# Performance work log

Hardware: AMD Instinct MI355X
Metric: run time of the kernel (lower is better)

Reference implementation:

```python
import jax, jax.numpy as jnp
import numpy as np

B, L, N = 4, 1024, 2048
V_DIM, L_DIM, HID, H = 512, 768, 512, 8
HD = HID // H
SCALE = HD ** -0.5


def setup_inputs() -> dict:
    key = jax.random.key(0)
    ks = jax.random.split(key, 6)
    return {
        "x": jax.random.normal(ks[0], (B, L, V_DIM), dtype=jnp.float32),
        "vfeats": jax.random.normal(ks[1], (B, N, L_DIM), dtype=jnp.float32),
        "topk_mask": jax.random.normal(ks[2], (B, H, L, N), dtype=jnp.float32),
        "Wq": jax.random.normal(ks[3], (HID, V_DIM), dtype=jnp.float32) * 0.02,
        "Wkv": jax.random.normal(ks[4], (2 * HID, L_DIM), dtype=jnp.float32) * 0.02,
        "Wproj": jax.random.normal(ks[5], (V_DIM, HID), dtype=jnp.float32) * 0.02,
        "bproj": jnp.zeros((V_DIM,), dtype=jnp.float32),
    }


def reference(x, vfeats, topk_mask, Wq, Wkv, Wproj, bproj):
    # q: [B,L,HID] -> [B,H,L,HD]
    q = (x @ Wq.T).reshape(B, L, H, HD).transpose(0, 2, 1, 3)
    # kv: [B,N,2*HID] -> k,v each [B,H,N,HD]
    kv = (vfeats @ Wkv.T).reshape(B, N, 2, H, HD).transpose(2, 0, 3, 1, 4)
    k, v = kv[0], kv[1]
    attn = jnp.einsum("bhld,bhnd->bhln", q, k) * SCALE + topk_mask
    attn = jax.nn.softmax(attn, axis=-1)
    out = jnp.einsum("bhln,bhnd->bhld", attn, v)  # [B,H,L,HD]
    out = out.transpose(0, 2, 1, 3).reshape(B, L, HID)
    return out @ Wproj.T + bproj
```

## Files before the change

kernel.cpp:

```cpp
#include <hip/hip_runtime.h>
#include <math.h>

#define B_ 4
#define L_ 1024
#define N_ 2048
#define VDIM_ 512
#define LDIM_ 768
#define HID_ 512
#define H_ 8
#define HD_ 64
#define SCALE_ 0.125f

typedef __bf16 bf16;
typedef __bf16 bf16x4 __attribute__((ext_vector_type(4)));
typedef __bf16 bf16x8 __attribute__((ext_vector_type(8)));
typedef float f32x4 __attribute__((ext_vector_type(4)));

__device__ __forceinline__ void async_cp16(const bf16* g, bf16* l) {
    __builtin_amdgcn_global_load_lds(
        (const __attribute__((address_space(1))) unsigned int*)g,
        (__attribute__((address_space(3))) unsigned int*)l, 16, 0, 0);
}

#define XE_   2097152
#define VFE_  6291456
#define WQE_  262144
#define WKVE_ 786432
__global__ void cvt_all(const float* __restrict__ x, const float* __restrict__ vf,
                        const float* __restrict__ wq, const float* __restrict__ wkv,
                        bf16* __restrict__ xb, bf16* __restrict__ vfb,
                        bf16* __restrict__ wqb, bf16* __restrict__ wkvb)
{
    int e = (blockIdx.x * 256 + threadIdx.x) * 4;
    const float* src; bf16* dst; int off;
    if (e < XE_)                        { src = x;   dst = xb;   off = 0; }
    else if (e < XE_ + VFE_)            { src = vf;  dst = vfb;  off = XE_; }
    else if (e < XE_ + VFE_ + WQE_)     { src = wq;  dst = wqb;  off = XE_ + VFE_; }
    else                                { src = wkv; dst = wkvb; off = XE_ + VFE_ + WQE_; }
    int i = e - off;
    float4 v = *(const float4*)(src + i);
    bf16x4 o;
    o[0] = (bf16)v.x; o[1] = (bf16)v.y; o[2] = (bf16)v.z; o[3] = (bf16)v.w;
    *(bf16x4*)(dst + i) = o;
}

__global__ void cvt_split(const float* __restrict__ in, bf16* __restrict__ hi,
                          bf16* __restrict__ lo, int n) {
    int i = (blockIdx.x * 256 + threadIdx.x) * 4;
    if (i < n) {
        float4 v = *(const float4*)(in + i);
        bf16x4 h, lw;
        float vv[4] = {v.x, v.y, v.z, v.w};
        #pragma unroll
        for (int j = 0; j < 4; ++j) {
            bf16 hb = (bf16)vv[j];
            h[j] = hb;
            lw[j] = (bf16)(vv[j] - (float)hb);
        }
        *(bf16x4*)(hi + i) = h;
        *(bf16x4*)(lo + i) = lw;
    }
}

template<int BM, int BN>
__global__ __launch_bounds__(256)
void gemm_bf16(const bf16* __restrict__ A, const bf16* __restrict__ W,
               bf16* __restrict__ C, int M, int N, int K)
{
    __shared__ bf16 As[BM * 64];
    __shared__ bf16 Ws[BN * 64];
    const int t = threadIdx.x, l = t & 63, wv = t >> 6;
    const int n0 = blockIdx.x * BN, m0 = blockIdx.y * BM;
    const int wm = (wv >> 1) * (BM / 2), wn = (wv & 1) * (BN / 2);
    constexpr int TI = BM / 32, TJ = BN / 32;
    const int lq = l & 15, qd = l >> 4, swz = l & 7;

    f32x4 acc[TI][TJ];
    #pragma unroll
    for (int i = 0; i < TI; ++i)
        #pragma unroll
        for (int j = 0; j < TJ; ++j)
            #pragma unroll
            for (int r = 0; r < 4; ++r) acc[i][j][r] = 0.f;

    for (int kt = 0; kt < K; kt += 64) {
        __syncthreads();
        for (int it = wv; it < BM / 8; it += 4) {
            int r = it * 8 + (l >> 3);
            int c = (l & 7) ^ (r & 7);
            async_cp16(A + (size_t)(m0 + r) * K + kt + c * 8, &As[it * 512]);
        }
        for (int it = wv; it < BN / 8; it += 4) {
            int r = it * 8 + (l >> 3);
            int c = (l & 7) ^ (r & 7);
            async_cp16(W + (size_t)(n0 + r) * K + kt + c * 8, &Ws[it * 512]);
        }
        __syncthreads();
        #pragma unroll
        for (int ks = 0; ks < 2; ++ks) {
            bf16x8 af[TI], wf[TJ];
            #pragma unroll
            for (int i = 0; i < TI; ++i) {
                int row = wm + i * 16 + lq;
                af[i] = *(const bf16x8*)&As[row * 64 + ((ks * 4 + qd) ^ swz) * 8];
            }
            #pragma unroll
            for (int j = 0; j < TJ; ++j) {
                int row = wn + j * 16 + lq;
                wf[j] = *(const bf16x8*)&Ws[row * 64 + ((ks * 4 + qd) ^ swz) * 8];
            }
            #pragma unroll
            for (int i = 0; i < TI; ++i)
                #pragma unroll
                for (int j = 0; j < TJ; ++j)
                    acc[i][j] = __builtin_amdgcn_mfma_f32_16x16x32_bf16(
                        af[i], wf[j], acc[i][j], 0, 0, 0);
        }
    }
    #pragma unroll
    for (int i = 0; i < TI; ++i)
        #pragma unroll
        for (int j = 0; j < TJ; ++j)
            #pragma unroll
            for (int r = 0; r < 4; ++r) {
                int row = m0 + wm + i * 16 + qd * 4 + r;
                int col = n0 + wn + j * 16 + lq;
                C[(size_t)row * N + col] = (bf16)acc[i][j][r];
            }
}

__global__ __launch_bounds__(256)
void gemm_proj(const bf16* __restrict__ A, const bf16* __restrict__ Wh,
               const bf16* __restrict__ Wl, const float* __restrict__ bias,
               float* __restrict__ Cf, int M, int N, int K)
{
    __shared__ bf16 sA[64 * 64];
    __shared__ bf16 sWh[64 * 64], sWl[64 * 64];
    const int t = threadIdx.x, l = t & 63, wv = t >> 6;
    const int n0 = blockIdx.x * 64, m0 = blockIdx.y * 64;
    const int wm = (wv >> 1) * 32, wn = (wv & 1) * 32;
    const int lq = l & 15, qd = l >> 4, swz = l & 7;

    f32x4 acc[2][2];
    #pragma unroll
    for (int i = 0; i < 2; ++i)
        #pragma unroll
        for (int j = 0; j < 2; ++j)
            #pragma unroll
            for (int r = 0; r < 4; ++r) acc[i][j][r] = 0.f;

    for (int kt = 0; kt < K; kt += 64) {
        __syncthreads();
        for (int it = wv; it < 8; it += 4) {
            int r = it * 8 + (l >> 3);
            int c = (l & 7) ^ (r & 7);
            async_cp16(A  + (size_t)(m0 + r) * K + kt + c * 8, &sA[it * 512]);
            size_t go = (size_t)(n0 + r) * K + kt + c * 8;
            async_cp16(Wh + go, &sWh[it * 512]);
            async_cp16(Wl + go, &sWl[it * 512]);
        }
        __syncthreads();
        #pragma unroll
        for (int ks = 0; ks < 2; ++ks) {
            bf16x8 af[2], wh[2], wl[2];
            #pragma unroll
            for (int i = 0; i < 2; ++i) {
                int off = (wm + i * 16 + lq) * 64 + ((ks * 4 + qd) ^ swz) * 8;
                af[i] = *(const bf16x8*)&sA[off];
            }
            #pragma unroll
            for (int j = 0; j < 2; ++j) {
                int off = (wn + j * 16 + lq) * 64 + ((ks * 4 + qd) ^ swz) * 8;
                wh[j] = *(const bf16x8*)&sWh[off];
                wl[j] = *(const bf16x8*)&sWl[off];
            }
            #pragma unroll
            for (int i = 0; i < 2; ++i)
                #pragma unroll
                for (int j = 0; j < 2; ++j) {
                    acc[i][j] = __builtin_amdgcn_mfma_f32_16x16x32_bf16(af[i], wh[j], acc[i][j], 0, 0, 0);
                    acc[i][j] = __builtin_amdgcn_mfma_f32_16x16x32_bf16(af[i], wl[j], acc[i][j], 0, 0, 0);
                }
        }
    }
    #pragma unroll
    for (int i = 0; i < 2; ++i)
        #pragma unroll
        for (int j = 0; j < 2; ++j) {
            int col = n0 + wn + j * 16 + lq;
            float bb = bias[col];
            #pragma unroll
            for (int r = 0; r < 4; ++r) {
                int row = m0 + wm + i * 16 + qd * 4 + r;
                Cf[(size_t)row * N + col] = acc[i][j][r] + bb;
            }
        }
}

__global__ __launch_bounds__(256)
void transpose_v(const bf16* __restrict__ kv, bf16* __restrict__ vT)
{
    __shared__ bf16 T[64 * 64];
    const int t = threadIdx.x;
    const int bid = blockIdx.x;
    const int nt = bid & 31, h = (bid >> 5) & 7, b = bid >> 8;
    const int n0 = nt * 64;
    for (int g = t; g < 512; g += 256) {
        int r = g >> 3, c = g & 7;
        bf16x8 v = *(const bf16x8*)(kv + (size_t)(b * N_ + n0 + r) * (2 * HID_) +
                                    HID_ + h * HD_ + c * 8);
        *(bf16x8*)&T[r * 64 + (c ^ (r & 7)) * 8] = v;
    }
    __syncthreads();
    for (int g = t; g < 512; g += 256) {
        int d = g >> 3, kg = g & 7;
        bf16x8 ov;
        #pragma unroll
        for (int jj = 0; jj < 8; ++jj) {
            int key = kg * 8 + jj;
            ov[jj] = T[key * 64 + (((d >> 3) ^ (key & 7))) * 8 + (d & 7)];
        }
        *(bf16x8*)&vT[(size_t)((b * H_ + h) * HD_ + d) * N_ + n0 + kg * 8] = ov;
    }
}

#define PST 136
__global__ __launch_bounds__(256)
void attn_mfma(const bf16* __restrict__ q, const bf16* __restrict__ kv,
               const bf16* __restrict__ vT, const float* __restrict__ mask,
               bf16* __restrict__ ao)
{
    __shared__ bf16 Ks[128 * 64];
    __shared__ bf16 Vs[64 * 128];
    __shared__ bf16 Pa[4][16 * PST];
    const int t = threadIdx.x, l = t & 63, wv = t >> 6;
    const int bid = blockIdx.x;
    const int lt = bid & 15, h = (bid >> 4) & 7, b = bid >> 7;
    const int l0 = lt * 64;
    const int lq = l & 15, qd = l >> 4, swz = l & 7;

    bf16x8 qf[2];
    {
        const bf16* qb = q + (size_t)(b * L_ + l0 + wv * 16 + lq) * HID_ + h * HD_ + qd * 8;
        qf[0] = *(const bf16x8*)qb;
        qf[1] = *(const bf16x8*)(qb + 32);
    }

    f32x4 o[4];
    #pragma unroll
    for (int j = 0; j < 4; ++j)
        #pragma unroll
        for (int r = 0; r < 4; ++r) o[j][r] = 0.f;
    float m_run[4], l_run[4];
    #pragma unroll
    for (int r = 0; r < 4; ++r) { m_run[r] = -1e30f; l_run[r] = 0.f; }

    const bf16* kb = kv + (size_t)(b * N_) * (2 * HID_) + h * HD_;
    const bf16* vb = vT + (size_t)((b * H_ + h) * HD_) * N_;
    const size_t mrow0 = (size_t)((b * H_ + h) * L_ + l0 + wv * 16);
    bf16* Paw = &Pa[wv][0];

    for (int nt = 0; nt < N_ / 128; ++nt) {
        const int n0 = nt * 128;
        __syncthreads();
        float mk[8][4];
        #pragma unroll
        for (int jj = 0; jj < 8; ++jj)
            #pragma unroll
            for (int r = 0; r < 4; ++r)
                mk[jj][r] = mask[(mrow0 + qd * 4 + r) * N_ + n0 + jj * 16 + lq];
        for (int it = wv; it < 16; it += 4) {
            int r = it * 8 + (l >> 3);
            int c = (l & 7) ^ (r & 7);
            async_cp16(kb + (size_t)(n0 + r) * (2 * HID_) + c * 8, &Ks[it * 512]);
        }
        for (int it = wv; it < 16; it += 4) {
            int r = it * 4 + (l >> 4);
            int c = (l & 15) ^ (r & 15);
            async_cp16(vb + (size_t)r * N_ + n0 + c * 8, &Vs[it * 512]);
        }
        __syncthreads();
        f32x4 s[8];
        #pragma unroll
        for (int jj = 0; jj < 8; ++jj)
            #pragma unroll
            for (int r = 0; r < 4; ++r) s[jj][r] = 0.f;
        #pragma unroll
        for (int ks = 0; ks < 2; ++ks)
            #pragma unroll
            for (int jj = 0; jj < 8; ++jj) {
                bf16x8 kf = *(const bf16x8*)&Ks[(jj * 16 + lq) * 64 +
                                                ((ks * 4 + qd) ^ swz) * 8];
                s[jj] = __builtin_amdgcn_mfma_f32_16x16x32_bf16(qf[ks], kf, s[jj], 0, 0, 0);
            }
        #pragma unroll
        for (int jj = 0; jj < 8; ++jj)
            #pragma unroll
            for (int r = 0; r < 4; ++r)
                s[jj][r] = fmaf(s[jj][r], SCALE_, mk[jj][r]);
        float alpha[4], mnew[4];
        #pragma unroll
        for (int r = 0; r < 4; ++r) {
            float mx = s[0][r];
            #pragma unroll
            for (int jj = 1; jj < 8; ++jj) mx = fmaxf(mx, s[jj][r]);
            #pragma unroll
            for (int d2 = 1; d2 < 16; d2 <<= 1) mx = fmaxf(mx, __shfl_xor(mx, d2));
            mnew[r] = fmaxf(m_run[r], mx);
            alpha[r] = __expf(m_run[r] - mnew[r]);
            m_run[r] = mnew[r];
        }
        bf16 pb[8][4];
        #pragma unroll
        for (int r = 0; r < 4; ++r) {
            float ss = 0.f;
            #pragma unroll
            for (int jj = 0; jj < 8; ++jj) {
                float p = __expf(s[jj][r] - mnew[r]);
                pb[jj][r] = (bf16)p;
                ss += p;
            }
            #pragma unroll
            for (int d2 = 1; d2 < 16; d2 <<= 1) ss += __shfl_xor(ss, d2);
            l_run[r] = l_run[r] * alpha[r] + ss;
        }
        #pragma unroll
        for (int jj = 0; jj < 8; ++jj)
            #pragma unroll
            for (int r = 0; r < 4; ++r)
                Paw[(qd * 4 + r) * PST + jj * 16 + lq] = pb[jj][r];
        __asm__ __volatile__("s_waitcnt lgkmcnt(0)" ::: "memory");
        #pragma unroll
        for (int jj = 0; jj < 4; ++jj)
            #pragma unroll
            for (int r = 0; r < 4; ++r) o[jj][r] *= alpha[r];
        #pragma unroll
        for (int ks = 0; ks < 4; ++ks) {
            bf16x8 pf = *(const bf16x8*)&Paw[lq * PST + ks * 32 + qd * 8];
            #pragma unroll
            for (int jj = 0; jj < 4; ++jj) {
                int d = jj * 16 + lq;
                bf16x8 vf = *(const bf16x8*)&Vs[d * 128 +
                                                ((ks * 4 + qd) ^ (d & 15)) * 8];
                o[jj] = __builtin_amdgcn_mfma_f32_16x16x32_bf16(pf, vf, o[jj], 0, 0, 0);
            }
        }
    }
    #pragma unroll
    for (int jj = 0; jj < 4; ++jj)
        #pragma unroll
        for (int r = 0; r < 4; ++r) {
            int row = b * L_ + l0 + wv * 16 + qd * 4 + r;
            int col = h * HD_ + jj * 16 + lq;
            ao[(size_t)row * HID_ + col] = (bf16)(o[jj][r] / l_run[r]);
        }
}

extern "C" void kernel_launch(void* const* d_in, const int* in_sizes, int n_in,
                              void* d_out, int out_size, void* d_ws, size_t ws_size,
                              hipStream_t stream)
{
    const float* x      = (const float*)d_in[0];
    const float* vfeats = (const float*)d_in[1];
    const float* mask   = (const float*)d_in[2];
    const float* Wq     = (const float*)d_in[3];
    const float* Wkv    = (const float*)d_in[4];
    const float* Wproj  = (const float*)d_in[5];
    const float* bproj  = (const float*)d_in[6];
    float* out = (float*)d_out;

    char* ws = (char*)d_ws;
    bf16* xb   = (bf16*)(ws);
    bf16* vfb  = (bf16*)(ws + 4194304);
    bf16* wqb  = (bf16*)(ws + 16777216);
    bf16* wkvb = (bf16*)(ws + 17301504);
    bf16* wph  = (bf16*)(ws + 18874368);
    bf16* wpl  = (bf16*)(ws + 19398656);
    bf16* qb   = (bf16*)(ws + 19922944);
    bf16* kvb  = (bf16*)(ws + 24117248);
    bf16* vTb  = (bf16*)(ws + 40894464);
    bf16* aob  = (bf16*)(ws + 49283072);

    dim3 blk(256);
    cvt_all<<<dim3((XE_ + VFE_ + WQE_ + WKVE_) / 1024), blk, 0, stream>>>(
        x, vfeats, Wq, Wkv, xb, vfb, wqb, wkvb);
    cvt_split<<<dim3(VDIM_ * HID_ / 1024), blk, 0, stream>>>(Wproj, wph, wpl, VDIM_ * HID_);
    gemm_bf16<64, 64><<<dim3(HID_ / 64, B_ * L_ / 64), blk, 0, stream>>>(
        xb, wqb, qb, B_ * L_, HID_, VDIM_);
    gemm_bf16<128, 64><<<dim3(2 * HID_ / 64, B_ * N_ / 128), blk, 0, stream>>>(
        vfb, wkvb, kvb, B_ * N_, 2 * HID_, LDIM_);
    transpose_v<<<dim3(B_ * H_ * (N_ / 64)), blk, 0, stream>>>(kvb, vTb);
    attn_mfma<<<dim3(B_ * H_ * (L_ / 64)), blk, 0, stream>>>(qb, kvb, vTb, mask, aob);
    gemm_proj<<<dim3(VDIM_ / 64, B_ * L_ / 64), blk, 0, stream>>>(
        aob, wph, wpl, bproj, out, B_ * L_, VDIM_, HID_);
}
```

Baseline: 453.1 us.

## Double-buffer attention K/V tiles with prefetched mask, fuse converts, widen KV GEMM tile

The attention kernel now uses 64-key tiles with double-buffered K/V shared memory and register-double-buffered mask loads, issuing the next tile's async copies before computing the current one. Waits are partial vmcnt counts plus raw barriers instead of full __syncthreads. This is meant to hide global-load latency behind MFMA work. The change also remaps block indices so neighbouring blocks share a head or batch differently, fuses the Wproj hi/lo split into the main convert kernel to save a launch, and widens the KV GEMM tile to 128x128. The hand-tuned vmcnt value and the pointer arithmetic add correctness and register-pressure risk.

```diff
diff --git a/kernel.cpp b/kernel.cpp
--- a/kernel.cpp
+++ b/kernel.cpp
@@ -26,39 +26,39 @@
 #define VFE_  6291456
 #define WQE_  262144
 #define WKVE_ 786432
+#define WPE_  262144
 __global__ void cvt_all(const float* __restrict__ x, const float* __restrict__ vf,
                         const float* __restrict__ wq, const float* __restrict__ wkv,
+                        const float* __restrict__ wp,
                         bf16* __restrict__ xb, bf16* __restrict__ vfb,
-                        bf16* __restrict__ wqb, bf16* __restrict__ wkvb)
+                        bf16* __restrict__ wqb, bf16* __restrict__ wkvb,
+                        bf16* __restrict__ wph, bf16* __restrict__ wpl)
 {
     int e = (blockIdx.x * 256 + threadIdx.x) * 4;
-    const float* src; bf16* dst; int off;
-    if (e < XE_)                        { src = x;   dst = xb;   off = 0; }
-    else if (e < XE_ + VFE_)            { src = vf;  dst = vfb;  off = XE_; }
-    else if (e < XE_ + VFE_ + WQE_)     { src = wq;  dst = wqb;  off = XE_ + VFE_; }
-    else                                { src = wkv; dst = wkvb; off = XE_ + VFE_ + WQE_; }
-    int i = e - off;
-    float4 v = *(const float4*)(src + i);
-    bf16x4 o;
-    o[0] = (bf16)v.x; o[1] = (bf16)v.y; o[2] = (bf16)v.z; o[3] = (bf16)v.w;
-    *(bf16x4*)(dst + i) = o;
-}
-
-__global__ void cvt_split(const float* __restrict__ in, bf16* __restrict__ hi,
-                          bf16* __restrict__ lo, int n) {
-    int i = (blockIdx.x * 256 + threadIdx.x) * 4;
-    if (i < n) {
-        float4 v = *(const float4*)(in + i);
-        bf16x4 h, lw;
+    if (e < XE_ + VFE_ + WQE_ + WKVE_) {
+        const float* src; bf16* dst; int off;
+        if (e < XE_)                        { src = x;   dst = xb;   off = 0; }
+        else if (e < XE_ + VFE_)            { src = vf;  dst = vfb;  off = XE_; }
+        else if (e < XE_ + VFE_ + WQE_)     { src = wq;  dst = wqb;  off = XE_ + VFE_; }
+        else                                { src = wkv; dst = wkvb; off = XE_ + VFE_ + WQE_; }
+        int i = e - off;
+        float4 v = *(const float4*)(src + i);
+        bf16x4 o;
+        o[0] = (bf16)v.x; o[1] = (bf16)v.y; o[2] = (bf16)v.z; o[3] = (bf16)v.w;
+        *(bf16x4*)(dst + i) = o;
+    } else {
+        int i = e - (XE_ + VFE_ + WQE_ + WKVE_);
+        float4 v = *(const float4*)(wp + i);
+        bf16x4 hh, ll;
         float vv[4] = {v.x, v.y, v.z, v.w};
         #pragma unroll
         for (int j = 0; j < 4; ++j) {
             bf16 hb = (bf16)vv[j];
-            h[j] = hb;
-            lw[j] = (bf16)(vv[j] - (float)hb);
-        }
-        *(bf16x4*)(hi + i) = h;
-        *(bf16x4*)(lo + i) = lw;
+            hh[j] = hb;
+            ll[j] = (bf16)(vv[j] - (float)hb);
+        }
+        *(bf16x4*)(wph + i) = hh;
+        *(bf16x4*)(wpl + i) = ll;
     }
 }
 
@@ -224,20 +224,25 @@
     }
 }
 
-#define PST 136
+#define KT_ 64
+#define NT_ 32
+#define PST 72
 __global__ __launch_bounds__(256)
 void attn_mfma(const bf16* __restrict__ q, const bf16* __restrict__ kv,
                const bf16* __restrict__ vT, const float* __restrict__ mask,
                bf16* __restrict__ ao)
 {
-    __shared__ bf16 Ks[128 * 64];
-    __shared__ bf16 Vs[64 * 128];
+    __shared__ bf16 Ks[2][64 * 64];
+    __shared__ bf16 Vs[2][64 * 64];
     __shared__ bf16 Pa[4][16 * PST];
     const int t = threadIdx.x, l = t & 63, wv = t >> 6;
-    const int bid = blockIdx.x;
+    const int bid0 = blockIdx.x;
+    const int bid = (bid0 & 7) * 64 + (bid0 >> 3);
     const int lt = bid & 15, h = (bid >> 4) & 7, b = bid >> 7;
     const int l0 = lt * 64;
     const int lq = l & 15, qd = l >> 4, swz = l & 7;
+    const int sr = l >> 3;
+    const int sc8 = ((l & 7) ^ sr) * 8;
 
     bf16x8 qf[2];
     {
@@ -260,92 +265,120 @@
     const size_t mrow0 = (size_t)((b * H_ + h) * L_ + l0 + wv * 16);
     bf16* Paw = &Pa[wv][0];
 
-    for (int nt = 0; nt < N_ / 128; ++nt) {
-        const int n0 = nt * 128;
-        __syncthreads();
-        float mk[8][4];
-        #pragma unroll
-        for (int jj = 0; jj < 8; ++jj)
-            #pragma unroll
-            for (int r = 0; r < 4; ++r)
-                mk[jj][r] = mask[(mrow0 + qd * 4 + r) * N_ + n0 + jj * 16 + lq];
-        for (int it = wv; it < 16; it += 4) {
-            int r = it * 8 + (l >> 3);
-            int c = (l & 7) ^ (r & 7);
-            async_cp16(kb + (size_t)(n0 + r) * (2 * HID_) + c * 8, &Ks[it * 512]);
-        }
-        for (int it = wv; it < 16; it += 4) {
-            int r = it * 4 + (l >> 4);
-            int c = (l & 15) ^ (r & 15);
-            async_cp16(vb + (size_t)r * N_ + n0 + c * 8, &Vs[it * 512]);
-        }
-        __syncthreads();
-        f32x4 s[8];
-        #pragma unroll
-        for (int jj = 0; jj < 8; ++jj)
-            #pragma unroll
-            for (int r = 0; r < 4; ++r) s[jj][r] = 0.f;
-        #pragma unroll
-        for (int ks = 0; ks < 2; ++ks)
-            #pragma unroll
-            for (int jj = 0; jj < 8; ++jj) {
-                bf16x8 kf = *(const bf16x8*)&Ks[(jj * 16 + lq) * 64 +
-                                                ((ks * 4 + qd) ^ swz) * 8];
-                s[jj] = __builtin_amdgcn_mfma_f32_16x16x32_bf16(qf[ks], kf, s[jj], 0, 0, 0);
-            }
-        #pragma unroll
-        for (int jj = 0; jj < 8; ++jj)
-            #pragma unroll
-            for (int r = 0; r < 4; ++r)
-                s[jj][r] = fmaf(s[jj][r], SCALE_, mk[jj][r]);
-        float alpha[4], mnew[4];
-        #pragma unroll
-        for (int r = 0; r < 4; ++r) {
-            float mx = s[0][r];
-            #pragma unroll
-            for (int jj = 1; jj < 8; ++jj) mx = fmaxf(mx, s[jj][r]);
-            #pragma unroll
-            for (int d2 = 1; d2 < 16; d2 <<= 1) mx = fmaxf(mx, __shfl_xor(mx, d2));
-            mnew[r] = fmaxf(m_run[r], mx);
-            alpha[r] = __expf(m_run[r] - mnew[r]);
-            m_run[r] = mnew[r];
-        }
-        bf16 pb[8][4];
-        #pragma unroll
-        for (int r = 0; r < 4; ++r) {
-            float ss = 0.f;
-            #pragma unroll
-            for (int jj = 0; jj < 8; ++jj) {
-                float p = __expf(s[jj][r] - mnew[r]);
-                pb[jj][r] = (bf16)p;
-                ss += p;
-            }
-            #pragma unroll
-            for (int d2 = 1; d2 < 16; d2 <<= 1) ss += __shfl_xor(ss, d2);
-            l_run[r] = l_run[r] * alpha[r] + ss;
-        }
-        #pragma unroll
-        for (int jj = 0; jj < 8; ++jj)
-            #pragma unroll
-            for (int r = 0; r < 4; ++r)
-                Paw[(qd * 4 + r) * PST + jj * 16 + lq] = pb[jj][r];
-        __asm__ __volatile__("s_waitcnt lgkmcnt(0)" ::: "memory");
-        #pragma unroll
-        for (int jj = 0; jj < 4; ++jj)
-            #pragma unroll
-            for (int r = 0; r < 4; ++r) o[jj][r] *= alpha[r];
-        #pragma unroll
-        for (int ks = 0; ks < 4; ++ks) {
-            bf16x8 pf = *(const bf16x8*)&Paw[lq * PST + ks * 32 + qd * 8];
-            #pragma unroll
-            for (int jj = 0; jj < 4; ++jj) {
-                int d = jj * 16 + lq;
-                bf16x8 vf = *(const bf16x8*)&Vs[d * 128 +
-                                                ((ks * 4 + qd) ^ (d & 15)) * 8];
-                o[jj] = __builtin_amdgcn_mfma_f32_16x16x32_bf16(pf, vf, o[jj], 0, 0, 0);
-            }
-        }
-    }
+    float mkA[4][4], mkB[4][4];
+
+#define STAGE(BUF, NTILE) do {                                                  \
+    const int nb_ = (NTILE) * KT_;                                              \
+    _Pragma("unroll")                                                           \
+    for (int it_ = 0; it_ < 2; ++it_) {                                         \
+        int r_ = (wv + it_ * 4) * 8 + sr;                                       \
+        async_cp16(kb + (size_t)(nb_ + r_) * (2 * HID_) + sc8,                  \
+                   &Ks[BUF][(wv + it_ * 4) * 512]);                             \
+    }                                                                           \
+    _Pragma("unroll")                                                           \
+    for (int it_ = 0; it_ < 2; ++it_) {                                         \
+        int r_ = (wv + it_ * 4) * 8 + sr;                                       \
+        async_cp16(vb + (size_t)r_ * N_ + nb_ + sc8,                            \
+                   &Vs[BUF][(wv + it_ * 4) * 512]);                             \
+    }                                                                           \
+} while (0)
+
+#define MASKLOAD(DST, NTILE) do {                                               \
+    const int nb_ = (NTILE) * KT_;                                              \
+    _Pragma("unroll")                                                           \
+    for (int jj = 0; jj < 4; ++jj)                                              \
+        _Pragma("unroll")                                                       \
+        for (int r = 0; r < 4; ++r)                                             \
+            DST[jj][r] = mask[(mrow0 + qd * 4 + r) * N_ + nb_ + jj * 16 + lq];  \
+} while (0)
+
+#define ATTN_ITER(NTI, CB, NB, MKC, MKN) do {                                   \
+    if ((NTI) + 1 < NT_) {                                                      \
+        STAGE(NB, (NTI) + 1);                                                   \
+        __builtin_amdgcn_sched_barrier(0);                                      \
+        MASKLOAD(MKN, (NTI) + 1);                                               \
+        __builtin_amdgcn_sched_barrier(0);                                      \
+    }                                                                           \
+                                              \
+    f32x4 s[4];                                                                 \
+    _Pragma("unroll")                                                           \
+    for (int jj = 0; jj < 4; ++jj)                                              \
+        _Pragma("unroll")                                                       \
+        for (int r = 0; r < 4; ++r) s[jj][r] = 0.f;                             \
+    _Pragma("unroll")                                                           \
+    for (int ks = 0; ks < 2; ++ks)                                              \
+        _Pragma("unroll")                                                       \
+        for (int jj = 0; jj < 4; ++jj) {                                        \
+            bf16x8 kf = *(const bf16x8*)&Ks[CB][(jj * 16 + lq) * 64 +           \
+                                               ((ks * 4 + qd) ^ swz) * 8];      \
+            s[jj] = __builtin_amdgcn_mfma_f32_16x16x32_bf16(qf[ks], kf, s[jj], 0, 0, 0); \
+        }                                                                       \
+    _Pragma("unroll")                                                           \
+    for (int jj = 0; jj < 4; ++jj)                                              \
+        _Pragma("unroll")                                                       \
+        for (int r = 0; r < 4; ++r)                                             \
+            s[jj][r] = fmaf(s[jj][r], SCALE_, MKC[jj][r]);                      \
+            \
+    float alpha[4], mnew[4];                                                    \
+    _Pragma("unroll")                                                           \
+    for (int r = 0; r < 4; ++r) {                                               \
+        float mx = fmaxf(fmaxf(s[0][r], s[1][r]), fmaxf(s[2][r], s[3][r]));     \
+        _Pragma("unroll")                                                       \
+        for (int d2 = 1; d2 < 16; d2 <<= 1) mx = fmaxf(mx, __shfl_xor(mx, d2)); \
+        mnew[r] = fmaxf(m_run[r], mx);                                          \
+        alpha[r] = __expf(m_run[r] - mnew[r]);                                  \
+        m_run[r] = mnew[r];                                                     \
+    }                                                                           \
+    _Pragma("unroll")                                                           \
+    for (int r = 0; r < 4; ++r) {                                               \
+        float ss = 0.f;                                                         \
+        _Pragma("unroll")                                                       \
+        for (int jj = 0; jj < 4; ++jj) {                                        \
+            float p = __expf(s[jj][r] - mnew[r]);                               \
+            Paw[(qd * 4 + r) * PST + jj * 16 + lq] = (bf16)p;                   \
+            ss += p;                                                            \
+        }                                                                       \
+        _Pragma("unroll")                                                       \
+        for (int d2 = 1; d2 < 16; d2 <<= 1) ss += __shfl_xor(ss, d2);           \
+        l_run[r] = l_run[r] * alpha[r] + ss;                                    \
+    }                                                                           \
+    asm volatile("s_waitcnt lgkmcnt(0)" ::: "memory");                          \
+    __builtin_amdgcn_sched_barrier(0);                                          \
+                                      \
+    _Pragma("unroll")                                                           \
+    for (int jj = 0; jj < 4; ++jj)                                              \
+        _Pragma("unroll")                                                       \
+        for (int r = 0; r < 4; ++r) o[jj][r] *= alpha[r];                       \
+    _Pragma("unroll")                                                           \
+    for (int ks = 0; ks < 2; ++ks) {                                            \
+        bf16x8 pf = *(const bf16x8*)&Paw[lq * PST + ks * 32 + qd * 8];          \
+        _Pragma("unroll")                                                       \
+        for (int jj = 0; jj < 4; ++jj) {                                        \
+            bf16x8 vf = *(const bf16x8*)&Vs[CB][(jj * 16 + lq) * 64 +           \
+                                               ((ks * 4 + qd) ^ swz) * 8];      \
+            o[jj] = __builtin_amdgcn_mfma_f32_16x16x32_bf16(pf, vf, o[jj], 0, 0, 0); \
+        }                                                                       \
+    }                                                                           \
+     \
+    __builtin_amdgcn_sched_barrier(0);                                          \
+    asm volatile("s_waitcnt vmcnt(16)" ::: "memory");                           \
+    __builtin_amdgcn_s_barrier();                                               \
+    __builtin_amdgcn_sched_barrier(0);                                          \
+} while (0)
+
+    STAGE(0, 0);
+    MASKLOAD(mkA, 0);
+    __syncthreads();
+
+    #pragma unroll 1
+    for (int nt2 = 0; nt2 < NT_; nt2 += 2) {
+        ATTN_ITER(nt2,     0, 1, mkA, mkB);
+        ATTN_ITER(nt2 + 1, 1, 0, mkB, mkA);
+    }
+#undef ATTN_ITER
+#undef MASKLOAD
+#undef STAGE
+
     #pragma unroll
     for (int jj = 0; jj < 4; ++jj)
         #pragma unroll
@@ -382,12 +415,11 @@
     bf16* aob  = (bf16*)(ws + 49283072);
 
     dim3 blk(256);
-    cvt_all<<<dim3((XE_ + VFE_ + WQE_ + WKVE_) / 1024), blk, 0, stream>>>(
-        x, vfeats, Wq, Wkv, xb, vfb, wqb, wkvb);
-    cvt_split<<<dim3(VDIM_ * HID_ / 1024), blk, 0, stream>>>(Wproj, wph, wpl, VDIM_ * HID_);
+    cvt_all<<<dim3((XE_ + VFE_ + WQE_ + WKVE_ + WPE_) / 1024), blk, 0, stream>>>(
+        x, vfeats, Wq, Wkv, Wproj, xb, vfb, wqb, wkvb, wph, wpl);
     gemm_bf16<64, 64><<<dim3(HID_ / 64, B_ * L_ / 64), blk, 0, stream>>>(
         xb, wqb, qb, B_ * L_, HID_, VDIM_);
-    gemm_bf16<128, 64><<<dim3(2 * HID_ / 64, B_ * N_ / 128), blk, 0, stream>>>(
+    gemm_bf16<128, 128><<<dim3(2 * HID_ / 128, B_ * N_ / 128), blk, 0, stream>>>(
         vfb, wkvb, kvb, B_ * N_, 2 * HID_, LDIM_);
     transpose_v<<<dim3(B_ * H_ * (N_ / 64)), blk, 0, stream>>>(kvb, vTb);
     attn_mfma<<<dim3(B_ * H_ * (L_ / 64)), blk, 0, stream>>>(qb, kvb, vTb, mask, aob);
```

New measurement: 452.8 us. About the same (-0.1%).
